# Optimization experiments

Hardware: AMD Instinct MI355X
Metric: run time of the kernel (lower is better)

The kernel has to match this reference:

```python
import jax, jax.numpy as jnp
import numpy as np

N_NODES = 50000
N_EDGES = 400000
D_PROT = 512
D_TEXT = 2048
GN_EPS = 1e-5


def setup_inputs() -> dict:
    key = jax.random.key(0)
    ks = jax.random.split(key, 8)
    s = 0.02
    return {
        "x": jax.random.normal(ks[0], (N_NODES, D_PROT), jnp.float32),
        "edge_index": jax.random.randint(ks[1], (2, N_EDGES), 0, N_NODES, dtype=jnp.int32),
        "gn_weight": jnp.ones((D_PROT,), jnp.float32),
        "gn_bias": jnp.zeros((D_PROT,), jnp.float32),
        "gn_mean_scale": jnp.ones((D_PROT,), jnp.float32),
        "conv1_w": jax.random.normal(ks[2], (D_PROT, D_PROT), jnp.float32) * s,
        "conv1_b": jnp.zeros((D_PROT,), jnp.float32),
        "conv2_w": jax.random.normal(ks[3], (D_PROT, D_PROT), jnp.float32) * s,
        "conv2_b": jnp.zeros((D_PROT,), jnp.float32),
        "proj1_w": jax.random.normal(ks[4], (D_TEXT, D_PROT), jnp.float32) * s,
        "proj1_b": jnp.zeros((D_TEXT,), jnp.float32),
        "proj2_w": jax.random.normal(ks[5], (D_TEXT, D_TEXT), jnp.float32) * s,
        "proj2_b": jnp.zeros((D_TEXT,), jnp.float32),
    }


def _graph_norm(x, weight, bias, mean_scale):
    # PyG GraphNorm over a single graph: shift by mean_scale*mean, scale by rstd
    mean = jnp.mean(x, axis=0, keepdims=True)            # [1, D]
    out = x - mean * mean_scale
    var = jnp.mean(out * out, axis=0, keepdims=True)     # [1, D]
    out = out * jax.lax.rsqrt(var + GN_EPS)
    return out * weight + bias


def _sgconv(x, src, dst, w, b):
    # SGConv K=1 with GCN normalization and added self-loops:
    n = x.shape[0]
    deg = jax.ops.segment_sum(jnp.ones_like(src, dtype=x.dtype), dst, num_segments=n) + 1.0
    dinv = jax.lax.rsqrt(deg)                            # [N]
    norm = dinv[src] * dinv[dst]                         # [E]
    agg = jax.ops.segment_sum(x[src] * norm[:, None], dst, num_segments=n)
    agg = agg + x * (dinv * dinv)[:, None]               # self-loop contribution
    return agg @ w.T + b


def reference(x, edge_index, gn_weight, gn_bias, gn_mean_scale,
              conv1_w, conv1_b, conv2_w, conv2_b,
              proj1_w, proj1_b, proj2_w, proj2_b):
    src, dst = edge_index[0], edge_index[1]
    h = _graph_norm(x, gn_weight, gn_bias, gn_mean_scale)
    h = jax.nn.relu(_sgconv(h, src, dst, conv1_w, conv1_b))  # dropout = identity (eval)
    h = jax.nn.relu(_sgconv(h, src, dst, conv2_w, conv2_b))
    h = h @ proj1_w.T + proj1_b
    h = jax.nn.gelu(h, approximate=False)
    h = h @ proj2_w.T + proj2_b
    return h
```

## Files before the change

kernel.cpp:

```cpp
#include <hip/hip_runtime.h>
#include <math.h>

typedef _Float16 half_t;
typedef _Float16 f16x2 __attribute__((ext_vector_type(2)));
typedef _Float16 f16x4 __attribute__((ext_vector_type(4)));
typedef _Float16 f16x8 __attribute__((ext_vector_type(8)));
typedef float f32x4 __attribute__((ext_vector_type(4)));

#define D_PROT 512
#define D_TEXT 2048

__global__ void k_cvt4(const float* __restrict__ s, half_t* __restrict__ d, int n4) {
    int i = blockIdx.x * 256 + threadIdx.x;
    if (i < n4) {
        float4 v = ((const float4*)s)[i];
        f16x4 o;
        o.x = (_Float16)v.x; o.y = (_Float16)v.y;
        o.z = (_Float16)v.z; o.w = (_Float16)v.w;
        ((f16x4*)d)[i] = o;
    }
}

__global__ void k_deg(const int* __restrict__ dst, int E, int* __restrict__ deg) {
    int i = blockIdx.x * 256 + threadIdx.x;
    if (i < E) atomicAdd(&deg[dst[i]], 1);
}

__global__ void k_dinv(const int* __restrict__ deg, float* __restrict__ dinv, int n) {
    int i = blockIdx.x * 256 + threadIdx.x;
    if (i < n) dinv[i] = rsqrtf((float)deg[i] + 1.0f);
}

__global__ void k_blocksum(const int* __restrict__ deg, int* __restrict__ bsum, int n) {
    __shared__ int sd[256];
    int i = blockIdx.x * 256 + threadIdx.x;
    sd[threadIdx.x] = (i < n) ? deg[i] : 0;
    __syncthreads();
    for (int s = 128; s > 0; s >>= 1) {
        if (threadIdx.x < s) sd[threadIdx.x] += sd[threadIdx.x + s];
        __syncthreads();
    }
    if (threadIdx.x == 0) bsum[blockIdx.x] = sd[0];
}

__global__ void k_scan_bsum(const int* __restrict__ bsum, int* __restrict__ boff, int nb) {
    if (threadIdx.x == 0 && blockIdx.x == 0) {
        int acc = 0;
        for (int i = 0; i < nb; i++) { boff[i] = acc; acc += bsum[i]; }
    }
}

__global__ void k_scan_final(const int* __restrict__ deg, const int* __restrict__ boff,
                             int* __restrict__ rowptr, int n) {
    __shared__ int sd[256];
    int i = blockIdx.x * 256 + threadIdx.x;
    int v = (i < n) ? deg[i] : 0;
    sd[threadIdx.x] = v;
    __syncthreads();
    for (int s = 1; s < 256; s <<= 1) {
        int t2 = (threadIdx.x >= s) ? sd[threadIdx.x - s] : 0;
        __syncthreads();
        sd[threadIdx.x] += t2;
        __syncthreads();
    }
    if (i < n) rowptr[i + 1] = boff[blockIdx.x] + sd[threadIdx.x];
}

__global__ void k_fill(const int* __restrict__ src, const int* __restrict__ dst, int E,
                       const int* __restrict__ rowptr, int* __restrict__ fill,
                       int* __restrict__ colidx) {
    int i = blockIdx.x * 256 + threadIdx.x;
    if (i < E) {
        int d = dst[i];
        int pos = atomicAdd(&fill[d], 1);
        colidx[rowptr[d] + pos] = src[i];
    }
}

__global__ void k_gnreduce(const float* __restrict__ x, float* __restrict__ sums,
                           float* __restrict__ sumsq, int Nn) {
    int t = threadIdx.x;
    int c = t * 2;
    float s0 = 0, s1 = 0, q0 = 0, q1 = 0;
    for (int r = blockIdx.x; r < Nn; r += gridDim.x) {
        float2 v = *(const float2*)(x + (size_t)r * D_PROT + c);
        s0 += v.x; s1 += v.y; q0 += v.x * v.x; q1 += v.y * v.y;
    }
    atomicAdd(&sums[c], s0);  atomicAdd(&sums[c + 1], s1);
    atomicAdd(&sumsq[c], q0); atomicAdd(&sumsq[c + 1], q1);
}

__global__ void k_gnfinal(const float* __restrict__ sums, const float* __restrict__ sumsq,
                          const float* __restrict__ w, const float* __restrict__ b,
                          const float* __restrict__ ms, float* __restrict__ ab, float invN) {
    int d = blockIdx.x * 256 + threadIdx.x;
    if (d < D_PROT) {
        float mean = sums[d] * invN;
        float m2 = sumsq[d] * invN;
        float mm = mean * ms[d];
        float var = m2 - 2.f * mm * mean + mm * mm;
        float rstd = rsqrtf(var + 1e-5f);
        float a = rstd * w[d];
        ab[d] = a;
        ab[D_PROT + d] = b[d] - mm * a;
    }
}

__global__ void k_gnnorm(const float* __restrict__ x, const float* __restrict__ ab,
                         half_t* __restrict__ h, int n4) {
    int i = blockIdx.x * 256 + threadIdx.x;
    if (i < n4) {
        size_t idx = (size_t)i * 4;
        float4 v = *(const float4*)(x + idx);
        int d = (int)(idx & (D_PROT - 1));
        const float* a = ab;
        const float* bb = ab + D_PROT;
        f16x4 o;
        o.x = (_Float16)(v.x * a[d]     + bb[d]);
        o.y = (_Float16)(v.y * a[d + 1] + bb[d + 1]);
        o.z = (_Float16)(v.z * a[d + 2] + bb[d + 2]);
        o.w = (_Float16)(v.w * a[d + 3] + bb[d + 3]);
        *(f16x4*)(h + idx) = o;
    }
}

__global__ void k_agg(const half_t* __restrict__ h, half_t* __restrict__ out,
                      const int* __restrict__ rowptr, const int* __restrict__ colidx,
                      const float* __restrict__ dinv) {
    int node = blockIdx.x;
    int t = threadIdx.x;
    float di = dinv[node];
    int beg = rowptr[node], end = rowptr[node + 1];
    f16x2 sv = ((const f16x2*)(h + (size_t)node * D_PROT))[t];
    float dii = di * di;
    float a0 = (float)sv.x * dii, a1 = (float)sv.y * dii;
    for (int e = beg; e < end; ++e) {
        int s = colidx[e];
        float wgt = dinv[s] * di;
        f16x2 v = ((const f16x2*)(h + (size_t)s * D_PROT))[t];
        a0 += wgt * (float)v.x;
        a1 += wgt * (float)v.y;
    }
    f16x2 o; o.x = (_Float16)a0; o.y = (_Float16)a1;
    ((f16x2*)(out + (size_t)node * D_PROT))[t] = o;
}

__device__ __forceinline__ void gload16(const half_t* g, half_t* l) {
    __builtin_amdgcn_global_load_lds(
        (const __attribute__((address_space(1))) void*)g,
        (__attribute__((address_space(3))) void*)l, 16, 0, 0);
}

template <int ACT, typename OUT_T>
__global__ __launch_bounds__(256) void k_gemm(const half_t* __restrict__ A,
                                              const half_t* __restrict__ W,
                                              const float* __restrict__ bias,
                                              OUT_T* __restrict__ C,
                                              int M, int N, int K) {
    __shared__ half_t lA[128 * 32];
    __shared__ half_t lB[128 * 32];
    const int bm = blockIdx.x * 128;
    const int bn = blockIdx.y * 128;
    const int t = threadIdx.x;
    const int lane = t & 63, wave = t >> 6;
    const int wm = (wave >> 1) * 64, wn = (wave & 1) * 64;
    const int fr = lane & 15, fq = lane >> 4;

    const int srow = t >> 2;
    const int scol = (t & 3) * 8;
    const half_t* gA0 = A + (size_t)min(bm + srow, M - 1) * K + scol;
    const half_t* gA1 = A + (size_t)min(bm + 64 + srow, M - 1) * K + scol;
    const half_t* gB0 = W + (size_t)(bn + srow) * K + scol;
    const half_t* gB1 = W + (size_t)(bn + 64 + srow) * K + scol;
    half_t* dA0 = &lA[wave * 512];
    half_t* dA1 = &lA[2048 + wave * 512];
    half_t* dB0 = &lB[wave * 512];
    half_t* dB1 = &lB[2048 + wave * 512];

    f32x4 acc[4][4] = {};

    for (int k0 = 0; k0 < K; k0 += 32) {
        __syncthreads();
        gload16(gA0 + k0, dA0);
        gload16(gA1 + k0, dA1);
        gload16(gB0 + k0, dB0);
        gload16(gB1 + k0, dB1);
        __syncthreads();
        f16x8 af[4], bf[4];
#pragma unroll
        for (int i = 0; i < 4; i++)
            af[i] = *(const f16x8*)&lA[(wm + i * 16 + fr) * 32 + fq * 8];
#pragma unroll
        for (int j = 0; j < 4; j++)
            bf[j] = *(const f16x8*)&lB[(wn + j * 16 + fr) * 32 + fq * 8];
#pragma unroll
        for (int i = 0; i < 4; i++)
#pragma unroll
            for (int j = 0; j < 4; j++)
                acc[i][j] = __builtin_amdgcn_mfma_f32_16x16x32_f16(af[i], bf[j], acc[i][j], 0, 0, 0);
    }

    const int col0 = bn + wn + fr;
#pragma unroll
    for (int i = 0; i < 4; i++) {
        int row_base = bm + wm + i * 16 + fq * 4;
#pragma unroll
        for (int j = 0; j < 4; j++) {
            int col = col0 + j * 16;
            float bv = bias[col];
#pragma unroll
            for (int r = 0; r < 4; r++) {
                int row = row_base + r;
                if (row < M) {
                    float v = acc[i][j][r] + bv;
                    if (ACT == 1) v = fmaxf(v, 0.f);
                    if (ACT == 2) v = 0.5f * v * (1.f + erff(v * 0.70710678118f));
                    C[(size_t)row * N + col] = (OUT_T)v;
                }
            }
        }
    }
}

#define FENCE() asm volatile("" ::: "memory")
#define BAR()   do { FENCE(); __builtin_amdgcn_s_barrier(); FENCE(); } while (0)
#define WAITV4() asm volatile("s_waitcnt vmcnt(4)" ::: "memory")
#define WAITV0() asm volatile("s_waitcnt vmcnt(0)" ::: "memory")
#define GLD(src, dst) __builtin_amdgcn_global_load_lds( \
    (const __attribute__((address_space(1))) void*)(src), \
    (__attribute__((address_space(3))) void*)(dst), 16, 0, 0)
#define LDF(base, row, kk) \
    (*(const f16x8*)((base) + ((((row) * 128 + (kk) * 64 + fqo)) ^ (((row) & 4) << 3))))
#define MM(mi, nj, A_, B_) \
    acc[mi][nj] = __builtin_amdgcn_mfma_f32_16x16x32_f16(A_, B_, acc[mi][nj], 0, 0, 0)

template <int ACT, typename OUT_T>
__global__ __launch_bounds__(512, 2) void k_gemm8(const half_t* __restrict__ A,
                                                  const half_t* __restrict__ W,
                                                  const float* __restrict__ bias,
                                                  OUT_T* __restrict__ C,
                                                  int M, int N, int K) {
    __shared__ half_t sm[2][32768];
    const int bn = blockIdx.x * 256;
    const int bm = blockIdx.y * 256;
    const int t = threadIdx.x;
    const int w = t >> 6, lane = t & 63;
    const int fr = lane & 15, fq = lane >> 4;
    const int fqo = fq * 16;
    const int wm = (w >> 2) * 128, wn = (w & 3) * 64;
    const int NT = K >> 6;

    int q0 = w * 512 + lane * 8;
    int q1 = 4096 + q0;
    int s0 = q0 ^ (((q0 >> 8) & 1) << 4);
    int s1 = q1 ^ (((q1 >> 8) & 1) << 4);
    int r0 = s0 >> 6, c0 = s0 & 63;
    int r1 = s1 >> 6, c1 = s1 & 63;
    const half_t* gAlo0 = A + (size_t)min(bm + r0, M - 1) * K + c0;
    const half_t* gAlo1 = A + (size_t)min(bm + r1, M - 1) * K + c1;
    const half_t* gAhi0 = A + (size_t)min(bm + 128 + r0, M - 1) * K + c0;
    const half_t* gAhi1 = A + (size_t)min(bm + 128 + r1, M - 1) * K + c1;
    const half_t* gBlo0 = W + (size_t)(bn + r0) * K + c0;
    const half_t* gBlo1 = W + (size_t)(bn + r1) * K + c1;
    const half_t* gBhi0 = W + (size_t)(bn + 128 + r0) * K + c0;
    const half_t* gBhi1 = W + (size_t)(bn + 128 + r1) * K + c1;
    const int dst0 = w * 512;

    f32x4 acc[8][4] = {};

    GLD(gAlo0, &sm[0][dst0]);          GLD(gAlo1, &sm[0][4096 + dst0]);
    GLD(gAhi0, &sm[0][8192 + dst0]);   GLD(gAhi1, &sm[0][12288 + dst0]);
    GLD(gBlo0, &sm[0][16384 + dst0]);  GLD(gBlo1, &sm[0][20480 + dst0]);
    GLD(gBhi0, &sm[0][24576 + dst0]);  GLD(gBhi1, &sm[0][28672 + dst0]);
    GLD(gBlo0 + 64, &sm[1][16384 + dst0]);  GLD(gBlo1 + 64, &sm[1][20480 + dst0]);
    GLD(gBhi0 + 64, &sm[1][24576 + dst0]);  GLD(gBhi1 + 64, &sm[1][28672 + dst0]);
    WAITV4();
    BAR();

#define TILE(cur, nxt, ktA, ktB) do {                                          \
    const char* smA = (const char*)&sm[cur][0];                                 \
    const char* smB = (const char*)&sm[cur][16384];                             \
                  \
    f16x8 b00 = LDF(smB, wn + fr, 0),      b01 = LDF(smB, wn + fr, 1);          \
    f16x8 b10 = LDF(smB, wn + 16 + fr, 0), b11 = LDF(smB, wn + 16 + fr, 1);     \
    f16x8 b20 = LDF(smB, wn + 32 + fr, 0), b21 = LDF(smB, wn + 32 + fr, 1);     \
    f16x8 b30 = LDF(smB, wn + 48 + fr, 0), b31 = LDF(smB, wn + 48 + fr, 1);     \
    f16x8 a00 = LDF(smA, wm + fr, 0),      a01 = LDF(smA, wm + fr, 1);          \
    f16x8 a10 = LDF(smA, wm + 16 + fr, 0), a11 = LDF(smA, wm + 16 + fr, 1);     \
    GLD(gAlo0 + (size_t)(ktA) * 64, &sm[nxt][dst0]);                            \
    GLD(gAlo1 + (size_t)(ktA) * 64, &sm[nxt][4096 + dst0]);                     \
    GLD(gAhi0 + (size_t)(ktA) * 64, &sm[nxt][8192 + dst0]);                     \
    GLD(gAhi1 + (size_t)(ktA) * 64, &sm[nxt][12288 + dst0]);                    \
    BAR();                                                                      \
    __builtin_amdgcn_s_setprio(1);                                              \
    MM(0, 0, a00, b00); MM(0, 1, a00, b10); MM(0, 2, a00, b20); MM(0, 3, a00, b30); \
    MM(0, 0, a01, b01); MM(0, 1, a01, b11); MM(0, 2, a01, b21); MM(0, 3, a01, b31); \
    MM(1, 0, a10, b00); MM(1, 1, a10, b10); MM(1, 2, a10, b20); MM(1, 3, a10, b30); \
    MM(1, 0, a11, b01); MM(1, 1, a11, b11); MM(1, 2, a11, b21); MM(1, 3, a11, b31); \
    __builtin_amdgcn_s_setprio(0);                                              \
    BAR();                                                                      \
                              \
    f16x8 a20 = LDF(smA, wm + 32 + fr, 0), a21 = LDF(smA, wm + 32 + fr, 1);     \
    f16x8 a30 = LDF(smA, wm + 48 + fr, 0), a31 = LDF(smA, wm + 48 + fr, 1);     \
    GLD(gBlo0 + (size_t)(ktB) * 64, &sm[cur][16384 + dst0]);                    \
    GLD(gBlo1 + (size_t)(ktB) * 64, &sm[cur][20480 + dst0]);                    \
    BAR();                                                                      \
    __builtin_amdgcn_s_setprio(1);                                              \
    MM(2, 0, a20, b00); MM(2, 1, a20, b10); MM(2, 2, a20, b20); MM(2, 3, a20, b30); \
    MM(2, 0, a21, b01); MM(2, 1, a21, b11); MM(2, 2, a21, b21); MM(2, 3, a21, b31); \
    MM(3, 0, a30, b00); MM(3, 1, a30, b10); MM(3, 2, a30, b20); MM(3, 3, a30, b30); \
    MM(3, 0, a31, b01); MM(3, 1, a31, b11); MM(3, 2, a31, b21); MM(3, 3, a31, b31); \
    __builtin_amdgcn_s_setprio(0);                                              \
    BAR();                                                                      \
                              \
    f16x8 a40 = LDF(smA, wm + 64 + fr, 0), a41 = LDF(smA, wm + 64 + fr, 1);     \
    f16x8 a50 = LDF(smA, wm + 80 + fr, 0), a51 = LDF(smA, wm + 80 + fr, 1);     \
    GLD(gBhi0 + (size_t)(ktB) * 64, &sm[cur][24576 + dst0]);                    \
    GLD(gBhi1 + (size_t)(ktB) * 64, &sm[cur][28672 + dst0]);                    \
    BAR();                                                                      \
    __builtin_amdgcn_s_setprio(1);                                              \
    MM(4, 0, a40, b00); MM(4, 1, a40, b10); MM(4, 2, a40, b20); MM(4, 3, a40, b30); \
    MM(4, 0, a41, b01); MM(4, 1, a41, b11); MM(4, 2, a41, b21); MM(4, 3, a41, b31); \
    MM(5, 0, a50, b00); MM(5, 1, a50, b10); MM(5, 2, a50, b20); MM(5, 3, a50, b30); \
    MM(5, 0, a51, b01); MM(5, 1, a51, b11); MM(5, 2, a51, b21); MM(5, 3, a51, b31); \
    __builtin_amdgcn_s_setprio(0);                                              \
    BAR();                                                                      \
                  \
    f16x8 a60 = LDF(smA, wm + 96 + fr, 0),  a61 = LDF(smA, wm + 96 + fr, 1);    \
    f16x8 a70 = LDF(smA, wm + 112 + fr, 0), a71 = LDF(smA, wm + 112 + fr, 1);   \
    BAR();                                                                      \
    __builtin_amdgcn_s_setprio(1);                                              \
    MM(6, 0, a60, b00); MM(6, 1, a60, b10); MM(6, 2, a60, b20); MM(6, 3, a60, b30); \
    MM(6, 0, a61, b01); MM(6, 1, a61, b11); MM(6, 2, a61, b21); MM(6, 3, a61, b31); \
    MM(7, 0, a70, b00); MM(7, 1, a70, b10); MM(7, 2, a70, b20); MM(7, 3, a70, b30); \
    MM(7, 0, a71, b01); MM(7, 1, a71, b11); MM(7, 2, a71, b21); MM(7, 3, a71, b31); \
    __builtin_amdgcn_s_setprio(0);                                              \
    WAITV4();                                                                   \
    BAR();                                                                      \
} while (0)

    for (int tt = 0; tt < NT; tt += 2) {
        int kb1 = (tt + 2 < NT) ? tt + 2 : NT - 1;
        TILE(0, 1, tt + 1, kb1);
        int ka2 = (tt + 2 < NT) ? tt + 2 : NT - 1;
        int kb2 = (tt + 3 < NT) ? tt + 3 : NT - 1;
        TILE(1, 0, ka2, kb2);
    }
    WAITV0();
#undef TILE

    const int col0 = bn + wn + fr;
#pragma unroll
    for (int mi = 0; mi < 8; mi++) {
        int rb = bm + wm + mi * 16 + fq * 4;
#pragma unroll
        for (int nj = 0; nj < 4; nj++) {
            int col = col0 + nj * 16;
            float bv = bias[col];
#pragma unroll
            for (int r = 0; r < 4; r++) {
                int row = rb + r;
                if (row < M) {
                    float v = acc[mi][nj][r] + bv;
                    if (ACT == 1) v = fmaxf(v, 0.f);
                    if (ACT == 2) v = 0.5f * v * (1.f + erff(v * 0.70710678118f));
                    C[(size_t)row * N + col] = (OUT_T)v;
                }
            }
        }
    }
}

extern "C" void kernel_launch(void* const* d_in, const int* in_sizes, int n_in,
                              void* d_out, int out_size, void* d_ws, size_t ws_size,
                              hipStream_t stream) {
    const float* x     = (const float*)d_in[0];
    const int*   eidx  = (const int*)d_in[1];
    const float* gn_w  = (const float*)d_in[2];
    const float* gn_b  = (const float*)d_in[3];
    const float* gn_ms = (const float*)d_in[4];
    const float* w1    = (const float*)d_in[5];
    const float* b1    = (const float*)d_in[6];
    const float* w2    = (const float*)d_in[7];
    const float* b2    = (const float*)d_in[8];
    const float* p1    = (const float*)d_in[9];
    const float* pb1   = (const float*)d_in[10];
    const float* p2    = (const float*)d_in[11];
    const float* pb2   = (const float*)d_in[12];

    const int Nn = in_sizes[0] / D_PROT;
    const int E  = in_sizes[1] / 2;
    const int M  = Nn;

    char* ws = (char*)d_ws;
    size_t off = 0;
    auto alloc = [&](size_t bytes) {
        void* p = ws + off;
        off += (bytes + 255) & ~(size_t)255;
        return p;
    };
    half_t* w1h    = (half_t*)alloc((size_t)D_PROT * D_PROT * 2);
    half_t* w2h    = (half_t*)alloc((size_t)D_PROT * D_PROT * 2);
    half_t* p1h    = (half_t*)alloc((size_t)D_TEXT * D_PROT * 2);
    half_t* p2h    = (half_t*)alloc((size_t)D_TEXT * D_TEXT * 2);
    int*    deg    = (int*)alloc((size_t)Nn * 4);
    float*  dinv   = (float*)alloc((size_t)Nn * 4);
    int*    rowptr = (int*)alloc((size_t)(Nn + 1) * 4);
    int*    fillc  = (int*)alloc((size_t)Nn * 4);
    int*    bsum   = (int*)alloc(1024);
    int*    boff   = (int*)alloc(1024);
    int*    colidx = (int*)alloc((size_t)E * 4);
    float*  sums   = (float*)alloc(D_PROT * 4);
    float*  sumsq  = (float*)alloc(D_PROT * 4);
    float*  gnab   = (float*)alloc(2 * D_PROT * 4);
    half_t* buf1   = (half_t*)alloc((size_t)Nn * D_PROT * 2);
    half_t* buf2   = (half_t*)alloc((size_t)Nn * D_PROT * 2);
    half_t* big    = (half_t*)alloc((size_t)Nn * D_TEXT * 2);

    const int* esrc = eidx;
    const int* edst = eidx + E;

    hipMemsetAsync(deg, 0, (size_t)Nn * 4, stream);
    hipMemsetAsync(fillc, 0, (size_t)Nn * 4, stream);
    hipMemsetAsync(rowptr, 0, (size_t)(Nn + 1) * 4, stream);
    hipMemsetAsync(sums, 0, D_PROT * 4, stream);
    hipMemsetAsync(sumsq, 0, D_PROT * 4, stream);

    k_cvt4<<<(D_PROT * D_PROT / 4 + 255) / 256, 256, 0, stream>>>(w1, w1h, D_PROT * D_PROT / 4);
    k_cvt4<<<(D_PROT * D_PROT / 4 + 255) / 256, 256, 0, stream>>>(w2, w2h, D_PROT * D_PROT / 4);
    k_cvt4<<<(D_TEXT * D_PROT / 4 + 255) / 256, 256, 0, stream>>>(p1, p1h, D_TEXT * D_PROT / 4);
    k_cvt4<<<(D_TEXT * D_TEXT / 4 + 255) / 256, 256, 0, stream>>>(p2, p2h, D_TEXT * D_TEXT / 4);

    int eb = (E + 255) / 256;
    int nb = (Nn + 255) / 256;
    k_deg<<<eb, 256, 0, stream>>>(edst, E, deg);
    k_dinv<<<nb, 256, 0, stream>>>(deg, dinv, Nn);
    k_blocksum<<<nb, 256, 0, stream>>>(deg, bsum, Nn);
    k_scan_bsum<<<1, 1, 0, stream>>>(bsum, boff, nb);
    k_scan_final<<<nb, 256, 0, stream>>>(deg, boff, rowptr, Nn);
    k_fill<<<eb, 256, 0, stream>>>(esrc, edst, E, rowptr, fillc, colidx);

    k_gnreduce<<<256, 256, 0, stream>>>(x, sums, sumsq, Nn);
    k_gnfinal<<<2, 256, 0, stream>>>(sums, sumsq, gn_w, gn_b, gn_ms, gnab, 1.0f / (float)Nn);
    int n4 = Nn * D_PROT / 4;
    k_gnnorm<<<(n4 + 255) / 256, 256, 0, stream>>>(x, gnab, buf1, n4);

    const int mt128 = (M + 127) / 128;
    const int mt256 = (M + 255) / 256;

    k_agg<<<Nn, 256, 0, stream>>>(buf1, buf2, rowptr, colidx, dinv);
    {
        dim3 g(mt128, D_PROT / 128);
        k_gemm<1, half_t><<<g, 256, 0, stream>>>(buf2, w1h, b1, buf1, M, D_PROT, D_PROT);
    }
    k_agg<<<Nn, 256, 0, stream>>>(buf1, buf2, rowptr, colidx, dinv);
    {
        dim3 g(mt128, D_PROT / 128);
        k_gemm<1, half_t><<<g, 256, 0, stream>>>(buf2, w2h, b2, buf1, M, D_PROT, D_PROT);
    }
    {
        dim3 g(D_TEXT / 256, mt256);
        k_gemm8<2, half_t><<<g, 512, 0, stream>>>(buf1, p1h, pb1, big, M, D_TEXT, D_PROT);
    }
    {
        dim3 g(D_TEXT / 256, mt256);
        k_gemm8<0, float><<<g, 512, 0, stream>>>(big, p2h, pb2, (float*)d_out, M, D_TEXT, D_TEXT);
    }
}
```

Before: 1.347 ms.

## Use pipelined 256x256 GEMM for SGConv layers, full LDS swizzle, XCD-aware block remap

Replaces the simple 128x128 single-buffered GEMM used for the two 512x512 SGConv projections with the double-buffered 256x256 k_gemm8 kernel. Changes the LDS XOR swizzle from a 1-bit pattern to a 3-bit row-based pattern to reduce bank conflicts on fragment reads. Adds a block-index remap that spreads consecutive workgroups across the eight XCDs when the grid size is divisible by 8. The larger tile gives fewer blocks for the small-N convolution GEMMs (2 column tiles), which may lower occupancy for those layers.

```diff
diff --git a/kernel.cpp b/kernel.cpp
--- a/kernel.cpp
+++ b/kernel.cpp
@@ -145,83 +145,6 @@
     ((f16x2*)(out + (size_t)node * D_PROT))[t] = o;
 }
 
-__device__ __forceinline__ void gload16(const half_t* g, half_t* l) {
-    __builtin_amdgcn_global_load_lds(
-        (const __attribute__((address_space(1))) void*)g,
-        (__attribute__((address_space(3))) void*)l, 16, 0, 0);
-}
-
-template <int ACT, typename OUT_T>
-__global__ __launch_bounds__(256) void k_gemm(const half_t* __restrict__ A,
-                                              const half_t* __restrict__ W,
-                                              const float* __restrict__ bias,
-                                              OUT_T* __restrict__ C,
-                                              int M, int N, int K) {
-    __shared__ half_t lA[128 * 32];
-    __shared__ half_t lB[128 * 32];
-    const int bm = blockIdx.x * 128;
-    const int bn = blockIdx.y * 128;
-    const int t = threadIdx.x;
-    const int lane = t & 63, wave = t >> 6;
-    const int wm = (wave >> 1) * 64, wn = (wave & 1) * 64;
-    const int fr = lane & 15, fq = lane >> 4;
-
-    const int srow = t >> 2;
-    const int scol = (t & 3) * 8;
-    const half_t* gA0 = A + (size_t)min(bm + srow, M - 1) * K + scol;
-    const half_t* gA1 = A + (size_t)min(bm + 64 + srow, M - 1) * K + scol;
-    const half_t* gB0 = W + (size_t)(bn + srow) * K + scol;
-    const half_t* gB1 = W + (size_t)(bn + 64 + srow) * K + scol;
-    half_t* dA0 = &lA[wave * 512];
-    half_t* dA1 = &lA[2048 + wave * 512];
-    half_t* dB0 = &lB[wave * 512];
-    half_t* dB1 = &lB[2048 + wave * 512];
-
-    f32x4 acc[4][4] = {};
-
-    for (int k0 = 0; k0 < K; k0 += 32) {
-        __syncthreads();
-        gload16(gA0 + k0, dA0);
-        gload16(gA1 + k0, dA1);
-        gload16(gB0 + k0, dB0);
-        gload16(gB1 + k0, dB1);
-        __syncthreads();
-        f16x8 af[4], bf[4];
-#pragma unroll
-        for (int i = 0; i < 4; i++)
-            af[i] = *(const f16x8*)&lA[(wm + i * 16 + fr) * 32 + fq * 8];
-#pragma unroll
-        for (int j = 0; j < 4; j++)
-            bf[j] = *(const f16x8*)&lB[(wn + j * 16 + fr) * 32 + fq * 8];
-#pragma unroll
-        for (int i = 0; i < 4; i++)
-#pragma unroll
-            for (int j = 0; j < 4; j++)
-                acc[i][j] = __builtin_amdgcn_mfma_f32_16x16x32_f16(af[i], bf[j], acc[i][j], 0, 0, 0);
-    }
-
-    const int col0 = bn + wn + fr;
-#pragma unroll
-    for (int i = 0; i < 4; i++) {
-        int row_base = bm + wm + i * 16 + fq * 4;
-#pragma unroll
-        for (int j = 0; j < 4; j++) {
-            int col = col0 + j * 16;
-            float bv = bias[col];
-#pragma unroll
-            for (int r = 0; r < 4; r++) {
-                int row = row_base + r;
-                if (row < M) {
-                    float v = acc[i][j][r] + bv;
-                    if (ACT == 1) v = fmaxf(v, 0.f);
-                    if (ACT == 2) v = 0.5f * v * (1.f + erff(v * 0.70710678118f));
-                    C[(size_t)row * N + col] = (OUT_T)v;
-                }
-            }
-        }
-    }
-}
-
 #define FENCE() asm volatile("" ::: "memory")
 #define BAR()   do { FENCE(); __builtin_amdgcn_s_barrier(); FENCE(); } while (0)
 #define WAITV4() asm volatile("s_waitcnt vmcnt(4)" ::: "memory")
@@ -230,7 +153,7 @@
     (const __attribute__((address_space(1))) void*)(src), \
     (__attribute__((address_space(3))) void*)(dst), 16, 0, 0)
 #define LDF(base, row, kk) \
-    (*(const f16x8*)((base) + ((((row) * 128 + (kk) * 64 + fqo)) ^ (((row) & 4) << 3))))
+    (*(const f16x8*)((base) + ((((row) * 128 + (kk) * 64 + fqo)) ^ (((row) & 7) << 4))))
 #define MM(mi, nj, A_, B_) \
     acc[mi][nj] = __builtin_amdgcn_mfma_f32_16x16x32_f16(A_, B_, acc[mi][nj], 0, 0, 0)
 
@@ -241,8 +164,13 @@
                                                   OUT_T* __restrict__ C,
                                                   int M, int N, int K) {
     __shared__ half_t sm[2][32768];
-    const int bn = blockIdx.x * 256;
-    const int bm = blockIdx.y * 256;
+    const int gx = gridDim.x;
+    const int nwg = gx * gridDim.y;
+    int b = blockIdx.y * gx + blockIdx.x;
+    int w8 = ((nwg & 7) == 0) ? (b & 7) * (nwg >> 3) + (b >> 3) : b;
+    const int bn = (w8 % gx) * 256;
+    const int bm = (w8 / gx) * 256;
+
     const int t = threadIdx.x;
     const int w = t >> 6, lane = t & 63;
     const int fr = lane & 15, fq = lane >> 4;
@@ -252,8 +180,8 @@
 
     int q0 = w * 512 + lane * 8;
     int q1 = 4096 + q0;
-    int s0 = q0 ^ (((q0 >> 8) & 1) << 4);
-    int s1 = q1 ^ (((q1 >> 8) & 1) << 4);
+    int s0 = q0 ^ (((q0 >> 6) & 7) << 3);
+    int s1 = q1 ^ (((q1 >> 6) & 7) << 3);
     int r0 = s0 >> 6, c0 = s0 & 63;
     int r1 = s1 >> 6, c1 = s1 & 63;
     const half_t* gAlo0 = A + (size_t)min(bm + r0, M - 1) * K + c0;
@@ -445,18 +373,17 @@
     int n4 = Nn * D_PROT / 4;
     k_gnnorm<<<(n4 + 255) / 256, 256, 0, stream>>>(x, gnab, buf1, n4);
 
-    const int mt128 = (M + 127) / 128;
     const int mt256 = (M + 255) / 256;
 
     k_agg<<<Nn, 256, 0, stream>>>(buf1, buf2, rowptr, colidx, dinv);
     {
-        dim3 g(mt128, D_PROT / 128);
-        k_gemm<1, half_t><<<g, 256, 0, stream>>>(buf2, w1h, b1, buf1, M, D_PROT, D_PROT);
+        dim3 g(D_PROT / 256, mt256);
+        k_gemm8<1, half_t><<<g, 512, 0, stream>>>(buf2, w1h, b1, buf1, M, D_PROT, D_PROT);
     }
     k_agg<<<Nn, 256, 0, stream>>>(buf1, buf2, rowptr, colidx, dinv);
     {
-        dim3 g(mt128, D_PROT / 128);
-        k_gemm<1, half_t><<<g, 256, 0, stream>>>(buf2, w2h, b2, buf1, M, D_PROT, D_PROT);
+        dim3 g(D_PROT / 256, mt256);
+        k_gemm8<1, half_t><<<g, 512, 0, stream>>>(buf2, w2h, b2, buf1, M, D_PROT, D_PROT);
     }
     {
         dim3 g(D_TEXT / 256, mt256);
```

New measurement: 1.321 ms. Within noise of the previous version (-1.9%).
